# Performance work log

Measured on AMD Instinct MI355X. Metric: run time of the kernel, lower is better.

The kernel has to match this reference:

```python
import jax, jax.numpy as jnp
import numpy as np

DIM = 512
HEADS = 8
HEAD_DIM = DIM // HEADS
SCALE = DIM ** (-0.5)  # source uses full dim, not head_dim
LAMBDA_COND = 1.0


def setup_inputs() -> dict:
    key = jax.random.key(0)
    ks = jax.random.split(key, 16)
    b, n, m_a, m_s = 4, 2048, 2048, 256
    s = 0.02
    inp = {
        "x": jax.random.normal(ks[0], (b, n, DIM), jnp.float32),
        "audio_context": jax.random.normal(ks[1], (b, m_a, DIM), jnp.float32),
        "singer_context": jax.random.normal(ks[2], (b, m_s, DIM), jnp.float32),
        "Wq": jax.random.normal(ks[3], (DIM, DIM), jnp.float32) * s,
        "bq": jnp.zeros((DIM,), jnp.float32),
        "Wka": jax.random.normal(ks[4], (DIM, DIM), jnp.float32) * s,
        "bka": jnp.zeros((DIM,), jnp.float32),
        "Wva": jax.random.normal(ks[5], (DIM, DIM), jnp.float32) * s,
        "bva": jnp.zeros((DIM,), jnp.float32),
        "Wks": jax.random.normal(ks[6], (DIM, DIM), jnp.float32) * s,
        "bks": jnp.zeros((DIM,), jnp.float32),
        "Wvs": jax.random.normal(ks[7], (DIM, DIM), jnp.float32) * s,
        "bvs": jnp.zeros((DIM,), jnp.float32),
        "Wp": jax.random.normal(ks[8], (DIM, DIM), jnp.float32) * s,
        "bp": jnp.zeros((DIM,), jnp.float32),
    }
    return inp


def _heads(t):
    b, n, c = t.shape
    return t.reshape(b, n, HEADS, HEAD_DIM).transpose(0, 2, 1, 3)  # (b,h,n,d)


def _attend(q, ctx, Wk, bk, Wv, bv):
    k = _heads(ctx @ Wk.T + bk)
    v = _heads(ctx @ Wv.T + bv)
    attn = jax.nn.softmax(jnp.einsum("bhnd,bhmd->bhnm", q, k) * SCALE, axis=-1)
    o = jnp.einsum("bhnm,bhmd->bhnd", attn, v)
    b, h, n, d = o.shape
    return o.transpose(0, 2, 1, 3).reshape(b, n, h * d)


def reference(x, audio_context, singer_context, Wq, bq, Wka, bka, Wva, bva,
              Wks, bks, Wvs, bvs, Wp, bp):
    q = _heads(x @ Wq.T + bq)
    x_audio = _attend(q, audio_context, Wka, bka, Wva, bva)
    x_singer = _attend(q, singer_context, Wks, bks, Wvs, bvs)
    out = x_audio + LAMBDA_COND * x_singer
    return out @ Wp.T + bp
```

## Files before the change

### kernel.cpp

```cpp
#include <hip/hip_runtime.h>

#define DIM 512
#define NQ 2048
#define MA 2048
#define MS 256
#define QSCALE 0.06375864651f

typedef __attribute__((ext_vector_type(8))) short bf16x8;
typedef __attribute__((ext_vector_type(4))) float f32x4;

__device__ __forceinline__ ushort f2b(float f) {
    uint u = __float_as_uint(f);
    u = (u + 0x7fffu + ((u >> 16) & 1u)) >> 16;
    return (ushort)u;
}

__device__ __forceinline__ void gload16(const ushort* g, ushort* l) {
    __builtin_amdgcn_global_load_lds(
        (const __attribute__((address_space(1))) void*)g,
        (__attribute__((address_space(3))) void*)l, 16, 0, 0);
}

__global__ __launch_bounds__(256) void cast_all(const float* __restrict__ w0,
                                                const float* __restrict__ w1,
                                                const float* __restrict__ w2,
                                                const float* __restrict__ w3,
                                                const float* __restrict__ w4,
                                                const float* __restrict__ w5,
                                                const float* __restrict__ x,
                                                const float* __restrict__ ac,
                                                const float* __restrict__ scx,
                                                ushort* __restrict__ dst) {
    int i = blockIdx.x * 256 + threadIdx.x;
    const float* s;
    int o;
    if (i < 393216) {
        int w = i >> 16;
        s = w < 3 ? (w == 0 ? w0 : (w == 1 ? w1 : w2))
                  : (w == 3 ? w3 : (w == 4 ? w4 : w5));
        o = i & 65535;
    } else if (i < 1441792) { s = x;   o = i - 393216; }
    else if (i < 2490368)   { s = ac;  o = i - 1441792; }
    else                    { s = scx; o = i - 2490368; }
    float4 v = ((const float4*)s)[o];
    ushort4 u;
    u.x = f2b(v.x); u.y = f2b(v.y); u.z = f2b(v.z); u.w = f2b(v.w);
    ((ushort4*)dst)[i] = u;
}

struct GD {
    const ushort* A; const ushort* B; const float* bias; void* out;
    long sB, sO;
    int N, bx, by, blk0, biasrow, scaleq, outf32, pad;
};

__global__ __launch_bounds__(256) void gemm_fused(GD d0, GD d1, GD d2, GD d3, GD d4) {
    __shared__ ushort At[128 * 32];
    __shared__ ushort Bt[128 * 32];
    GD d = d0;
    int bid = blockIdx.x;
    if (bid >= d1.blk0) d = d1;
    if (bid >= d2.blk0) d = d2;
    if (bid >= d3.blk0) d = d3;
    if (bid >= d4.blk0) d = d4;
    int local = bid - d.blk0;
    int x = local % d.bx;
    int rem = local / d.bx;
    int y = rem % d.by;
    int z = rem / d.by;

    int t = threadIdx.x;
    int wv = t >> 6, ln = t & 63, l = ln & 15, g = ln >> 4;
    int wrow = wv & 1, wcol = wv >> 1;
    int row0 = x * 128, col0 = y * 128;
    int srow = t >> 2;
    int slot = (t & 3) * 8;
    int sko = ((t ^ srow) & 3) * 8;
    int kc8 = ((g ^ (l & 3)) & 3) * 8;
    const ushort* Ab = d.A;
    const ushort* Bb = d.B + (size_t)z * d.sB;
    int N = d.N;

    f32x4 acc[4][4];
#pragma unroll
    for (int i = 0; i < 4; i++)
#pragma unroll
        for (int j = 0; j < 4; j++) acc[i][j] = (f32x4){0, 0, 0, 0};

    for (int k0 = 0; k0 < 512; k0 += 32) {
        __syncthreads();
#pragma unroll
        for (int c = 0; c < 2; c++) {
            gload16(Ab + (size_t)(row0 + srow + 64 * c) * 512 + k0 + sko,
                    At + (srow + 64 * c) * 32 + slot);
            gload16(Bb + (size_t)(col0 + srow + 64 * c) * 512 + k0 + sko,
                    Bt + (srow + 64 * c) * 32 + slot);
        }
        __syncthreads();
        bf16x8 ar[4], br[4];
#pragma unroll
        for (int i = 0; i < 4; i++)
            ar[i] = *(const bf16x8*)(At + (wrow * 64 + i * 16 + l) * 32 + kc8);
#pragma unroll
        for (int j = 0; j < 4; j++)
            br[j] = *(const bf16x8*)(Bt + (wcol * 64 + j * 16 + l) * 32 + kc8);
#pragma unroll
        for (int i = 0; i < 4; i++)
#pragma unroll
            for (int j = 0; j < 4; j++)
                acc[i][j] = __builtin_amdgcn_mfma_f32_16x16x32_bf16(ar[i], br[j], acc[i][j], 0, 0, 0);
    }
#pragma unroll
    for (int i = 0; i < 4; i++) {
#pragma unroll
        for (int j = 0; j < 4; j++) {
            int row = row0 + wrow * 64 + i * 16 + g * 4;
            int col = col0 + wcol * 64 + j * 16 + l;
#pragma unroll
            for (int r = 0; r < 4; r++) {
                float bv = d.biasrow ? d.bias[row + r] : d.bias[col];
                float o = acc[i][j][r] + bv;
                if (d.scaleq) o *= QSCALE;
                if (d.outf32)
                    ((float*)d.out + (size_t)z * d.sO)[(size_t)(row + r) * N + col] = o;
                else
                    ((ushort*)d.out + (size_t)z * d.sO)[(size_t)(row + r) * N + col] = f2b(o);
            }
        }
    }
}

__device__ __forceinline__ void attn_ctx(const ushort* __restrict__ kg,
                                         const ushort* __restrict__ vg,
                                         int M, const bf16x8 (&aq)[2],
                                         ushort* __restrict__ Kl,
                                         ushort* __restrict__ Vl,
                                         ushort* __restrict__ Pw,
                                         f32x4 (&acc)[4], float& li,
                                         int l, int g, int sr, int sc) {
    bf16x8 k = *(const bf16x8*)kg;
    bf16x8 v = *(const bf16x8*)vg;
    for (int mt = 0; mt < M; mt += 64) {
        __syncthreads();
        *(bf16x8*)(Kl + sr * 72 + sc) = k;
        *(bf16x8*)(Vl + sr * 72 + sc) = v;
        __syncthreads();
        if (mt + 64 < M) {
            k = *(const bf16x8*)(kg + (size_t)(mt + 64) * DIM);
            v = *(const bf16x8*)(vg + (mt + 64));
        }
#pragma unroll
        for (int tt = 0; tt < 4; tt++) {
            bf16x8 kb0 = *(const bf16x8*)(Kl + (16 * tt + l) * 72 + g * 8);
            bf16x8 kb1 = *(const bf16x8*)(Kl + (16 * tt + l) * 72 + 32 + g * 8);
            f32x4 s = {0, 0, 0, 0};
            s = __builtin_amdgcn_mfma_f32_16x16x32_bf16(kb0, aq[0], s, 0, 0, 0);
            s = __builtin_amdgcn_mfma_f32_16x16x32_bf16(kb1, aq[1], s, 0, 0, 0);
            float p0 = exp2f(s[0]), p1 = exp2f(s[1]);
            float p2 = exp2f(s[2]), p3 = exp2f(s[3]);
            li += (p0 + p1) + (p2 + p3);
            uint u0 = (__float_as_uint(p0) + 0x8000u) >> 16;
            uint u1 = (__float_as_uint(p1) + 0x8000u) >> 16;
            uint u2 = (__float_as_uint(p2) + 0x8000u) >> 16;
            uint u3 = (__float_as_uint(p3) + 0x8000u) >> 16;
            uint2 pw;
            pw.x = u0 | (u1 << 16);
            pw.y = u2 | (u3 << 16);
            *(uint2*)(Pw + l * 72 + 16 * tt + g * 4) = pw;
        }
        bf16x8 pa0 = *(const bf16x8*)(Pw + l * 72 + g * 8);
        bf16x8 pa1 = *(const bf16x8*)(Pw + l * 72 + 32 + g * 8);
#pragma unroll
        for (int c = 0; c < 4; c++) {
            bf16x8 vb0 = *(const bf16x8*)(Vl + (c * 16 + l) * 72 + g * 8);
            bf16x8 vb1 = *(const bf16x8*)(Vl + (c * 16 + l) * 72 + 32 + g * 8);
            acc[c] = __builtin_amdgcn_mfma_f32_16x16x32_bf16(pa0, vb0, acc[c], 0, 0, 0);
            acc[c] = __builtin_amdgcn_mfma_f32_16x16x32_bf16(pa1, vb1, acc[c], 0, 0, 0);
        }
    }
}

__global__ __launch_bounds__(512) void attn_kernel(const ushort* __restrict__ q,
                                                   const ushort* __restrict__ Ka,
                                                   const ushort* __restrict__ VTa,
                                                   const ushort* __restrict__ Ks,
                                                   const ushort* __restrict__ VTs,
                                                   ushort* __restrict__ y) {
    __shared__ ushort Kl[64 * 72];
    __shared__ ushort Vl[64 * 72];
    __shared__ ushort Pl[8 * 16 * 72];
    int t = threadIdx.x;
    int wv = t >> 6, ln = t & 63, l = ln & 15, g = ln >> 4;
    int h = blockIdx.y, bi = blockIdx.z;
    int q0 = blockIdx.x * 128 + wv * 16;
    bf16x8 aq[2];
    aq[0] = *(const bf16x8*)(q + (size_t)(bi * NQ + q0 + l) * DIM + h * 64 + g * 8);
    aq[1] = *(const bf16x8*)(q + (size_t)(bi * NQ + q0 + l) * DIM + h * 64 + 32 + g * 8);
    int sr = t >> 3, sc = (t & 7) * 8;
    ushort* Pw = Pl + wv * 16 * 72;

    f32x4 acc[4];
    float li = 0.f;
#pragma unroll
    for (int c = 0; c < 4; c++) acc[c] = (f32x4){0, 0, 0, 0};

    {
        const ushort* kg = Ks + (size_t)bi * MS * DIM + (size_t)sr * DIM + h * 64 + sc;
        const ushort* vg = VTs + (size_t)bi * DIM * MS + (size_t)(h * 64 + sr) * MS + sc;
        attn_ctx(kg, vg, MS, aq, Kl, Vl, Pw, acc, li, l, g, sr, sc);
    }
    li += __shfl_xor(li, 16);
    li += __shfl_xor(li, 32);
    float yv[4][4];
    float inv[4];
#pragma unroll
    for (int r = 0; r < 4; r++) inv[r] = 1.f / __shfl(li, g * 4 + r);
#pragma unroll
    for (int c = 0; c < 4; c++)
#pragma unroll
        for (int r = 0; r < 4; r++) yv[c][r] = acc[c][r] * inv[r];

#pragma unroll
    for (int c = 0; c < 4; c++) acc[c] = (f32x4){0, 0, 0, 0};
    li = 0.f;
    {
        const ushort* kg = Ka + (size_t)bi * MA * DIM + (size_t)sr * DIM + h * 64 + sc;
        const ushort* vg = VTa + (size_t)bi * DIM * MA + (size_t)(h * 64 + sr) * MA + sc;
        attn_ctx(kg, vg, MA, aq, Kl, Vl, Pw, acc, li, l, g, sr, sc);
    }
    li += __shfl_xor(li, 16);
    li += __shfl_xor(li, 32);
#pragma unroll
    for (int r = 0; r < 4; r++) inv[r] = 1.f / __shfl(li, g * 4 + r);
#pragma unroll
    for (int c = 0; c < 4; c++)
#pragma unroll
        for (int r = 0; r < 4; r++) {
            float o = yv[c][r] + acc[c][r] * inv[r];
            y[(size_t)(bi * NQ + q0 + g * 4 + r) * DIM + h * 64 + c * 16 + l] = f2b(o);
        }
}

extern "C" void kernel_launch(void* const* d_in, const int* in_sizes, int n_in,
                              void* d_out, int out_size, void* d_ws, size_t ws_size,
                              hipStream_t stream) {
    const float* x   = (const float*)d_in[0];
    const float* ac  = (const float*)d_in[1];
    const float* scx = (const float*)d_in[2];
    const float* Wq  = (const float*)d_in[3];
    const float* bq  = (const float*)d_in[4];
    const float* Wka = (const float*)d_in[5];
    const float* bka = (const float*)d_in[6];
    const float* Wva = (const float*)d_in[7];
    const float* bva = (const float*)d_in[8];
    const float* Wks = (const float*)d_in[9];
    const float* bks = (const float*)d_in[10];
    const float* Wvs = (const float*)d_in[11];
    const float* bvs = (const float*)d_in[12];
    const float* Wp  = (const float*)d_in[13];
    const float* bp  = (const float*)d_in[14];

    ushort* wb   = (ushort*)d_ws;
    ushort* wqb  = wb;
    ushort* wkab = wb + 262144;
    ushort* wvab = wb + 2 * 262144;
    ushort* wksb = wb + 3 * 262144;
    ushort* wvsb = wb + 4 * 262144;
    ushort* wpb  = wb + 5 * 262144;
    ushort* xb   = wb + 6 * 262144;
    ushort* acb  = xb + 4194304;
    ushort* scxb = acb + 4194304;
    ushort* qb   = scxb + 524288;
    ushort* kab  = qb + 4194304;
    ushort* vta  = kab + 4194304;
    ushort* ksb  = vta + 4194304;
    ushort* vts  = ksb + 524288;
    ushort* yb   = xb;

    cast_all<<<10240, 256, 0, stream>>>(Wq, Wka, Wva, Wks, Wvs, Wp, x, ac, scx, wb);

    GD gq   = {xb,   wqb,  bq,  qb,  0, 0,               512,  64, 4,  0,   0, 1, 0, 0};
    GD gka  = {acb,  wkab, bka, kab, 0, 0,               512,  64, 4,  256, 0, 0, 0, 0};
    GD gvta = {wvab, acb,  bva, vta, 2048L * 512, 512L * 2048, 2048, 4, 16, 512, 1, 0, 0, 0};
    GD gks  = {scxb, wksb, bks, ksb, 0, 0,               512,  8,  4,  768, 0, 0, 0, 0};
    GD gvts = {wvsb, scxb, bvs, vts, 256L * 512, 512L * 256,   256,  4,  2,  800, 1, 0, 0, 0};
    gemm_fused<<<832, 256, 0, stream>>>(gq, gka, gvta, gks, gvts);

    attn_kernel<<<dim3(16, 8, 4), 512, 0, stream>>>(qb, kab, vta, ksb, vts, yb);

    GD gpr = {yb, wpb, bp, d_out, 0, 0, 512, 64, 4, 0, 0, 0, 1, 0};
    GD gnv = {nullptr, nullptr, nullptr, nullptr, 0, 0, 0, 1, 1, 1 << 30, 0, 0, 0, 0};
    gemm_fused<<<256, 256, 0, stream>>>(gpr, gnv, gnv, gnv, gnv);
}
```

Measured before the change: 246.1 us.

## Switch attention to 32x32x16 MFMA with 32 query rows per wave

The attention kernel now uses 32x32x16 bf16 MFMA tiles in place of 16x16x32, so each wave handles 32 query rows instead of 16. The block drops from 512 to 256 threads while keeping 128 queries per block, and each thread stages two K/V rows per tile into LDS. The aim is fewer MFMA issues and fewer LDS fragment reads per unit of work, giving more reuse per wave. The cost is higher register pressure from the 16-wide accumulators and the 32-entry yv array, and fewer waves per block to hide latency.

```diff
diff --git a/kernel.cpp b/kernel.cpp
--- a/kernel.cpp
+++ b/kernel.cpp
@@ -8,6 +8,7 @@
 
 typedef __attribute__((ext_vector_type(8))) short bf16x8;
 typedef __attribute__((ext_vector_type(4))) float f32x4;
+typedef __attribute__((ext_vector_type(16))) float f32x16;
 
 __device__ __forceinline__ ushort f2b(float f) {
     uint u = __float_as_uint(f);
@@ -130,57 +131,71 @@
     }
 }
 
-__device__ __forceinline__ void attn_ctx(const ushort* __restrict__ kg,
-                                         const ushort* __restrict__ vg,
-                                         int M, const bf16x8 (&aq)[2],
-                                         ushort* __restrict__ Kl,
-                                         ushort* __restrict__ Vl,
-                                         ushort* __restrict__ Pw,
-                                         f32x4 (&acc)[4], float& li,
-                                         int l, int g, int sr, int sc) {
-    bf16x8 k = *(const bf16x8*)kg;
-    bf16x8 v = *(const bf16x8*)vg;
+__device__ __forceinline__ void attn_ctx32(const ushort* __restrict__ kg,
+                                           const ushort* __restrict__ vg,
+                                           int M, const bf16x8 (&aq)[4],
+                                           ushort* __restrict__ Kl,
+                                           ushort* __restrict__ Vl,
+                                           ushort* __restrict__ Pw,
+                                           f32x16 (&o)[2], float& li,
+                                           int l5, int hi, int sr, int sc) {
+    bf16x8 k0 = *(const bf16x8*)kg;
+    bf16x8 k1 = *(const bf16x8*)(kg + (size_t)32 * DIM);
+    bf16x8 v0 = *(const bf16x8*)vg;
+    bf16x8 v1 = *(const bf16x8*)(vg + (size_t)32 * M);
     for (int mt = 0; mt < M; mt += 64) {
         __syncthreads();
-        *(bf16x8*)(Kl + sr * 72 + sc) = k;
-        *(bf16x8*)(Vl + sr * 72 + sc) = v;
+        *(bf16x8*)(Kl + sr * 72 + sc) = k0;
+        *(bf16x8*)(Kl + (sr + 32) * 72 + sc) = k1;
+        *(bf16x8*)(Vl + sr * 72 + sc) = v0;
+        *(bf16x8*)(Vl + (sr + 32) * 72 + sc) = v1;
         __syncthreads();
         if (mt + 64 < M) {
-            k = *(const bf16x8*)(kg + (size_t)(mt + 64) * DIM);
-            v = *(const bf16x8*)(vg + (mt + 64));
-        }
-#pragma unroll
-        for (int tt = 0; tt < 4; tt++) {
-            bf16x8 kb0 = *(const bf16x8*)(Kl + (16 * tt + l) * 72 + g * 8);
-            bf16x8 kb1 = *(const bf16x8*)(Kl + (16 * tt + l) * 72 + 32 + g * 8);
-            f32x4 s = {0, 0, 0, 0};
-            s = __builtin_amdgcn_mfma_f32_16x16x32_bf16(kb0, aq[0], s, 0, 0, 0);
-            s = __builtin_amdgcn_mfma_f32_16x16x32_bf16(kb1, aq[1], s, 0, 0, 0);
-            float p0 = exp2f(s[0]), p1 = exp2f(s[1]);
-            float p2 = exp2f(s[2]), p3 = exp2f(s[3]);
-            li += (p0 + p1) + (p2 + p3);
-            uint u0 = (__float_as_uint(p0) + 0x8000u) >> 16;
-            uint u1 = (__float_as_uint(p1) + 0x8000u) >> 16;
-            uint u2 = (__float_as_uint(p2) + 0x8000u) >> 16;
-            uint u3 = (__float_as_uint(p3) + 0x8000u) >> 16;
-            uint2 pw;
-            pw.x = u0 | (u1 << 16);
-            pw.y = u2 | (u3 << 16);
-            *(uint2*)(Pw + l * 72 + 16 * tt + g * 4) = pw;
-        }
-        bf16x8 pa0 = *(const bf16x8*)(Pw + l * 72 + g * 8);
-        bf16x8 pa1 = *(const bf16x8*)(Pw + l * 72 + 32 + g * 8);
-#pragma unroll
-        for (int c = 0; c < 4; c++) {
-            bf16x8 vb0 = *(const bf16x8*)(Vl + (c * 16 + l) * 72 + g * 8);
-            bf16x8 vb1 = *(const bf16x8*)(Vl + (c * 16 + l) * 72 + 32 + g * 8);
-            acc[c] = __builtin_amdgcn_mfma_f32_16x16x32_bf16(pa0, vb0, acc[c], 0, 0, 0);
-            acc[c] = __builtin_amdgcn_mfma_f32_16x16x32_bf16(pa1, vb1, acc[c], 0, 0, 0);
-        }
+            k0 = *(const bf16x8*)(kg + (size_t)(mt + 64) * DIM);
+            k1 = *(const bf16x8*)(kg + (size_t)(mt + 96) * DIM);
+            v0 = *(const bf16x8*)(vg + (mt + 64));
+            v1 = *(const bf16x8*)(vg + (size_t)32 * M + (mt + 64));
+        }
+#pragma unroll
+        for (int c = 0; c < 2; c++) {
+            f32x16 s;
+#pragma unroll
+            for (int i = 0; i < 16; i++) s[i] = 0.f;
+#pragma unroll
+            for (int kd = 0; kd < 4; kd++) {
+                bf16x8 kf = *(const bf16x8*)(Kl + (32 * c + l5) * 72 + kd * 16 + hi * 8);
+                s = __builtin_amdgcn_mfma_f32_32x32x16_bf16(kf, aq[kd], s, 0, 0, 0);
+            }
+#pragma unroll
+            for (int m = 0; m < 4; m++) {
+                float p0 = exp2f(s[4 * m + 0]);
+                float p1 = exp2f(s[4 * m + 1]);
+                float p2 = exp2f(s[4 * m + 2]);
+                float p3 = exp2f(s[4 * m + 3]);
+                li += (p0 + p1) + (p2 + p3);
+                uint2 pw;
+                pw.x = ((__float_as_uint(p0) + 0x8000u) >> 16) |
+                       ((__float_as_uint(p1) + 0x8000u) & 0xffff0000u);
+                pw.y = ((__float_as_uint(p2) + 0x8000u) >> 16) |
+                       ((__float_as_uint(p3) + 0x8000u) & 0xffff0000u);
+                *(uint2*)(Pw + l5 * 72 + 32 * c + 8 * m + 4 * hi) = pw;
+            }
+        }
+        bf16x8 pf[4];
+#pragma unroll
+        for (int kc = 0; kc < 4; kc++)
+            pf[kc] = *(const bf16x8*)(Pw + l5 * 72 + kc * 16 + hi * 8);
+#pragma unroll
+        for (int dn = 0; dn < 2; dn++)
+#pragma unroll
+            for (int kc = 0; kc < 4; kc++) {
+                bf16x8 vf = *(const bf16x8*)(Vl + (32 * dn + l5) * 72 + kc * 16 + hi * 8);
+                o[dn] = __builtin_amdgcn_mfma_f32_32x32x16_bf16(pf[kc], vf, o[dn], 0, 0, 0);
+            }
     }
 }
 
-__global__ __launch_bounds__(512) void attn_kernel(const ushort* __restrict__ q,
+__global__ __launch_bounds__(256) void attn_kernel(const ushort* __restrict__ q,
                                                    const ushort* __restrict__ Ka,
                                                    const ushort* __restrict__ VTa,
                                                    const ushort* __restrict__ Ks,
@@ -188,56 +203,59 @@
                                                    ushort* __restrict__ y) {
     __shared__ ushort Kl[64 * 72];
     __shared__ ushort Vl[64 * 72];
-    __shared__ ushort Pl[8 * 16 * 72];
+    __shared__ ushort Pl[4 * 32 * 72];
     int t = threadIdx.x;
-    int wv = t >> 6, ln = t & 63, l = ln & 15, g = ln >> 4;
+    int wv = t >> 6, ln = t & 63, l5 = ln & 31, hi = ln >> 5;
     int h = blockIdx.y, bi = blockIdx.z;
-    int q0 = blockIdx.x * 128 + wv * 16;
-    bf16x8 aq[2];
-    aq[0] = *(const bf16x8*)(q + (size_t)(bi * NQ + q0 + l) * DIM + h * 64 + g * 8);
-    aq[1] = *(const bf16x8*)(q + (size_t)(bi * NQ + q0 + l) * DIM + h * 64 + 32 + g * 8);
+    int q0 = blockIdx.x * 128 + wv * 32;
+    bf16x8 aq[4];
+    const ushort* qp = q + (size_t)(bi * NQ + q0 + l5) * DIM + h * 64 + hi * 8;
+#pragma unroll
+    for (int kd = 0; kd < 4; kd++) aq[kd] = *(const bf16x8*)(qp + kd * 16);
     int sr = t >> 3, sc = (t & 7) * 8;
-    ushort* Pw = Pl + wv * 16 * 72;
-
-    f32x4 acc[4];
+    ushort* Pw = Pl + wv * 32 * 72;
+
+    f32x16 o[2];
+#pragma unroll
+    for (int dn = 0; dn < 2; dn++)
+#pragma unroll
+        for (int i = 0; i < 16; i++) o[dn][i] = 0.f;
     float li = 0.f;
-#pragma unroll
-    for (int c = 0; c < 4; c++) acc[c] = (f32x4){0, 0, 0, 0};
-
-    {
-        const ushort* kg = Ks + (size_t)bi * MS * DIM + (size_t)sr * DIM + h * 64 + sc;
-        const ushort* vg = VTs + (size_t)bi * DIM * MS + (size_t)(h * 64 + sr) * MS + sc;
-        attn_ctx(kg, vg, MS, aq, Kl, Vl, Pw, acc, li, l, g, sr, sc);
-    }
-    li += __shfl_xor(li, 16);
+
+    attn_ctx32(Ks + (size_t)bi * MS * DIM + (size_t)sr * DIM + h * 64 + sc,
+               VTs + (size_t)bi * DIM * MS + (size_t)(h * 64 + sr) * MS + sc,
+               MS, aq, Kl, Vl, Pw, o, li, l5, hi, sr, sc);
     li += __shfl_xor(li, 32);
-    float yv[4][4];
-    float inv[4];
-#pragma unroll
-    for (int r = 0; r < 4; r++) inv[r] = 1.f / __shfl(li, g * 4 + r);
-#pragma unroll
-    for (int c = 0; c < 4; c++)
-#pragma unroll
-        for (int r = 0; r < 4; r++) yv[c][r] = acc[c][r] * inv[r];
-
-#pragma unroll
-    for (int c = 0; c < 4; c++) acc[c] = (f32x4){0, 0, 0, 0};
+    float inv[16];
+#pragma unroll
+    for (int rg = 0; rg < 16; rg++)
+        inv[rg] = 1.f / __shfl(li, (rg & 3) + 8 * (rg >> 2) + 4 * hi);
+    float yv[2][16];
+#pragma unroll
+    for (int dn = 0; dn < 2; dn++)
+#pragma unroll
+        for (int rg = 0; rg < 16; rg++) yv[dn][rg] = o[dn][rg] * inv[rg];
+
+#pragma unroll
+    for (int dn = 0; dn < 2; dn++)
+#pragma unroll
+        for (int i = 0; i < 16; i++) o[dn][i] = 0.f;
     li = 0.f;
-    {
-        const ushort* kg = Ka + (size_t)bi * MA * DIM + (size_t)sr * DIM + h * 64 + sc;
-        const ushort* vg = VTa + (size_t)bi * DIM * MA + (size_t)(h * 64 + sr) * MA + sc;
-        attn_ctx(kg, vg, MA, aq, Kl, Vl, Pw, acc, li, l, g, sr, sc);
-    }
-    li += __shfl_xor(li, 16);
+    attn_ctx32(Ka + (size_t)bi * MA * DIM + (size_t)sr * DIM + h * 64 + sc,
+               VTa + (size_t)bi * DIM * MA + (size_t)(h * 64 + sr) * MA + sc,
+               MA, aq, Kl, Vl, Pw, o, li, l5, hi, sr, sc);
     li += __shfl_xor(li, 32);
 #pragma unroll
-    for (int r = 0; r < 4; r++) inv[r] = 1.f / __shfl(li, g * 4 + r);
-#pragma unroll
-    for (int c = 0; c < 4; c++)
-#pragma unroll
-        for (int r = 0; r < 4; r++) {
-            float o = yv[c][r] + acc[c][r] * inv[r];
-            y[(size_t)(bi * NQ + q0 + g * 4 + r) * DIM + h * 64 + c * 16 + l] = f2b(o);
+    for (int rg = 0; rg < 16; rg++)
+        inv[rg] = 1.f / __shfl(li, (rg & 3) + 8 * (rg >> 2) + 4 * hi);
+
+#pragma unroll
+    for (int dn = 0; dn < 2; dn++)
+#pragma unroll
+        for (int rg = 0; rg < 16; rg++) {
+            int qr = (rg & 3) + 8 * (rg >> 2) + 4 * hi;
+            float ov = yv[dn][rg] + o[dn][rg] * inv[rg];
+            y[(size_t)(bi * NQ + q0 + qr) * DIM + h * 64 + 32 * dn + l5] = f2b(ov);
         }
 }
 
@@ -286,7 +304,7 @@
     GD gvts = {wvsb, scxb, bvs, vts, 256L * 512, 512L * 256,   256,  4,  2,  800, 1, 0, 0, 0};
     gemm_fused<<<832, 256, 0, stream>>>(gq, gka, gvta, gks, gvts);
 
-    attn_kernel<<<dim3(16, 8, 4), 512, 0, stream>>>(qb, kab, vta, ksb, vts, yb);
+    attn_kernel<<<dim3(16, 8, 4), 256, 0, stream>>>(qb, kab, vta, ksb, vts, yb);
 
     GD gpr = {yb, wpb, bp, d_out, 0, 0, 512, 64, 4, 0, 0, 0, 1, 0};
     GD gnv = {nullptr, nullptr, nullptr, nullptr, 0, 0, 0, 1, 1, 1 << 30, 0, 0, 0, 0};
```

Measured after the change: 252.8 us. 2.7% more time.
